# Kernel tuning notes

Measured on AMD Instinct MI355X. Metric: run time of the kernel, lower is better.

The kernel has to match this reference:

```python
import jax, jax.numpy as jnp
import numpy as np

D_MODEL = 512
H = 8
DEPTH = D_MODEL // H
TOPK = 16
TAU_HID = max(4, D_MODEL // 2)  # 256
TAU_EPS = 1e-6
DT = 1.0
T_SCALAR = 1.0  # default t in call()


def setup_inputs() -> dict:
    key = jax.random.key(0)
    ks = jax.random.split(key, 24)
    B, T = 2, 1024
    D2 = 2 * DEPTH

    def w(k, shape, fan_in):
        return jax.random.normal(k, shape, dtype=jnp.float32) / np.sqrt(fan_in)

    inp = {
        "x": jax.random.normal(ks[0], (B, T, D_MODEL), dtype=jnp.float32),
        "Wq": w(ks[1], (D_MODEL, D_MODEL), D_MODEL), "bq": jnp.zeros((D_MODEL,), jnp.float32),
        "Wk": w(ks[2], (D_MODEL, D_MODEL), D_MODEL), "bk": jnp.zeros((D_MODEL,), jnp.float32),
        "Wv": w(ks[3], (D_MODEL, D_MODEL), D_MODEL), "bv": jnp.zeros((D_MODEL,), jnp.float32),
        "Wo": w(ks[4], (D_MODEL, D_MODEL), D_MODEL), "bo": jnp.zeros((D_MODEL,), jnp.float32),
        "Wpi": w(ks[5], (D2, D_MODEL), D2), "bpi": jnp.zeros((D_MODEL,), jnp.float32),
        "Wpo": w(ks[6], (D_MODEL, 1), D_MODEL), "bpo": jnp.zeros((1,), jnp.float32),
        "Wta": w(ks[7], (D2, 1), D2), "bta": jnp.zeros((1,), jnp.float32),
        "Wtb": w(ks[8], (D2, 1), D2), "btb": jnp.zeros((1,), jnp.float32),
        "Wti": w(ks[9], (D2, TAU_HID), D2), "bti": jnp.zeros((TAU_HID,), jnp.float32),
        "Wto": w(ks[10], (TAU_HID, 1), TAU_HID), "bto": jnp.zeros((1,), jnp.float32),
    }
    return inp


def reference(x, Wq, bq, Wk, bk, Wv, bv, Wo, bo,
              Wpi, bpi, Wpo, bpo, Wta, bta, Wtb, btb, Wti, bti, Wto, bto):
    B, T, _ = x.shape

    def split_heads(z):
        return z.reshape(B, T, H, DEPTH).transpose(0, 2, 1, 3)  # [B,H,T,D]

    qh = split_heads(x @ Wq + bq)
    kh = split_heads(x @ Wk + bk)
    vh = split_heads(x @ Wv + bv)

    # top-k pairwise scores (q @ k^T), select K keys per query
    scores = jnp.einsum('bhqd,bhkd->bhqk', qh, kh)  # [B,H,T,T]
    _, idx = jax.lax.top_k(scores, TOPK)            # [B,H,T,K]

    # gather k and v at top-k indices -> [B,H,T,K,D]
    kg = jnp.take_along_axis(kh[:, :, None, :, :], idx[..., None], axis=3)
    vg = jnp.take_along_axis(vh[:, :, None, :, :], idx[..., None], axis=3)

    # per-pair features [q_i ; k_j] -> [B,H,T,K,2D]
    qt = jnp.broadcast_to(qh[:, :, :, None, :], (B, H, T, TOPK, DEPTH))
    pairs = jnp.concatenate([qt, kg], axis=-1)

    # phi: Dense(d_model) -> Dense(1) -> sigmoid
    phi = jax.nn.sigmoid(((pairs @ Wpi + bpi) @ Wpo + bpo)[..., 0])
    # time interpolation: sigmoid(a*t + b)
    t_a = (pairs @ Wta + bta)[..., 0]
    t_b = (pairs @ Wtb + btb)[..., 0]
    t_interp = jax.nn.sigmoid(t_a * T_SCALAR + t_b)
    # tau: Dense(d_model//2) -> Dense(1) -> softplus + eps
    tau = jax.nn.softplus(((pairs @ Wti + bti) @ Wto + bto)[..., 0]) + TAU_EPS

    # mode == 'exact'
    attn_logits = phi / tau * (1.0 - jnp.exp(-tau * t_interp))
    attn = jax.nn.softmax(attn_logits, axis=-1)  # [B,H,T,K]

    out_h = jnp.einsum('bhqk,bhqkd->bhqd', attn, vg) * DT  # [B,H,T,D]
    combined = out_h.transpose(0, 2, 1, 3).reshape(B, T, D_MODEL)
    return combined @ Wo + bo  # return_sequences=True
```

## Files before the change

### kernel.cpp

```cpp
#include <hip/hip_runtime.h>
#include <math.h>

#define BDIM 2
#define TT 1024
#define NH 8
#define HD 64
#define NTOPK 16
#define NBH 16
#define NTOK 16384

__global__ __launch_bounds__(256) void k_collapse64(
    const float* __restrict__ Wpi, const float* __restrict__ bpi,
    const float* __restrict__ Wpo, const float* __restrict__ bpo,
    const float* __restrict__ Wti, const float* __restrict__ bti,
    const float* __restrict__ Wto, const float* __restrict__ bto,
    double* __restrict__ wphid, double* __restrict__ wtaud,
    double* __restrict__ ccd) {
  int tid = threadIdx.x;
  int blk = blockIdx.x;
  if (blk < 16) {
    int r = blk * 16 + (tid >> 4);
    int l = tid & 15;
    double s = 0.;
    if (r < 128) {
      for (int i = 0; i < 32; ++i)
        s += (double)Wpi[r * 512 + l + 16 * i] * (double)Wpo[l + 16 * i];
    } else {
      int rr = r - 128;
      for (int i = 0; i < 16; ++i)
        s += (double)Wti[rr * 256 + l + 16 * i] * (double)Wto[l + 16 * i];
    }
#pragma unroll
    for (int off = 8; off >= 1; off >>= 1) s += __shfl_xor(s, off, 64);
    if (l == 0) {
      if (r < 128) wphid[r] = s;
      else wtaud[r - 128] = s;
    }
  } else {
    int lane = tid & 63;
    if (tid < 64) {
      double p = 0.;
      for (int c = lane; c < 512; c += 64) p += (double)bpi[c] * (double)Wpo[c];
#pragma unroll
      for (int off = 32; off >= 1; off >>= 1) p += __shfl_xor(p, off, 64);
      if (lane == 0) ccd[0] = p + (double)bpo[0];
    } else if (tid < 128) {
      double p = 0.;
      for (int c = lane; c < 256; c += 64) p += (double)bti[c] * (double)Wto[c];
#pragma unroll
      for (int off = 32; off >= 1; off >>= 1) p += __shfl_xor(p, off, 64);
      if (lane == 0) ccd[1] = p + (double)bto[0];
    }
  }
}

__device__ __forceinline__ void gemm_body(
    const float* __restrict__ A, const float* __restrict__ W,
    const float* __restrict__ bias, float* __restrict__ out,
    int bm, int bn, int mode) {
  __shared__ float As[16][64];
  __shared__ float Bs[16][64];
  const int tid = threadIdx.x;
  const int tx = tid & 15;
  const int ty = tid >> 4;
  const int lr = tid >> 2;
  const int lc = (tid & 3) << 2;
  float acc[4][4] = {{0.f, 0.f, 0.f, 0.f}};
  for (int k0 = 0; k0 < 512; k0 += 16) {
    float4 av = *(const float4*)&A[(bm + lr) * 512 + k0 + lc];
    As[lc + 0][lr] = av.x;
    As[lc + 1][lr] = av.y;
    As[lc + 2][lr] = av.z;
    As[lc + 3][lr] = av.w;
    *(float4*)&Bs[ty][tx << 2] = *(const float4*)&W[(k0 + ty) * 512 + bn + (tx << 2)];
    __syncthreads();
#pragma unroll
    for (int kk = 0; kk < 16; ++kk) {
      float4 a = *(const float4*)&As[kk][ty * 4];
      float4 b = *(const float4*)&Bs[kk][tx << 2];
      acc[0][0] = fmaf(a.x, b.x, acc[0][0]);
      acc[0][1] = fmaf(a.x, b.y, acc[0][1]);
      acc[0][2] = fmaf(a.x, b.z, acc[0][2]);
      acc[0][3] = fmaf(a.x, b.w, acc[0][3]);
      acc[1][0] = fmaf(a.y, b.x, acc[1][0]);
      acc[1][1] = fmaf(a.y, b.y, acc[1][1]);
      acc[1][2] = fmaf(a.y, b.z, acc[1][2]);
      acc[1][3] = fmaf(a.y, b.w, acc[1][3]);
      acc[2][0] = fmaf(a.z, b.x, acc[2][0]);
      acc[2][1] = fmaf(a.z, b.y, acc[2][1]);
      acc[2][2] = fmaf(a.z, b.z, acc[2][2]);
      acc[2][3] = fmaf(a.z, b.w, acc[2][3]);
      acc[3][0] = fmaf(a.w, b.x, acc[3][0]);
      acc[3][1] = fmaf(a.w, b.y, acc[3][1]);
      acc[3][2] = fmaf(a.w, b.z, acc[3][2]);
      acc[3][3] = fmaf(a.w, b.w, acc[3][3]);
    }
    __syncthreads();
  }
#pragma unroll
  for (int i = 0; i < 4; ++i) {
    int row = bm + ty * 4 + i;
    float4 r;
    r.x = acc[i][0] + bias[bn + tx * 4 + 0];
    r.y = acc[i][1] + bias[bn + tx * 4 + 1];
    r.z = acc[i][2] + bias[bn + tx * 4 + 2];
    r.w = acc[i][3] + bias[bn + tx * 4 + 3];
    if (mode == 0) {
      *(float4*)&out[row * 512 + bn + tx * 4] = r;
    } else {
      int bb = row >> 10;
      int tt2 = row & 1023;
      int head = bn >> 6;
      *(float4*)&out[(((bb * NH + head) * TT + tt2) << 6) + tx * 4] = r;
    }
  }
}

__global__ __launch_bounds__(256) void k_gemm(
    const float* __restrict__ A, const float* __restrict__ W,
    const float* __restrict__ bias, float* __restrict__ out, int mode) {
  gemm_body(A, W, bias, out, blockIdx.y * 64, blockIdx.x * 64, mode);
}

__global__ __launch_bounds__(256) void k_gemm_qkv(
    const float* __restrict__ A,
    const float* __restrict__ Wq, const float* __restrict__ bq,
    const float* __restrict__ Wk, const float* __restrict__ bk,
    const float* __restrict__ Wv, const float* __restrict__ bv,
    float* __restrict__ Qf, float* __restrict__ Kf, float* __restrict__ Vf) {
  int which = blockIdx.x >> 3;
  int bn = (blockIdx.x & 7) * 64;
  const float* W = (which == 0) ? Wq : (which == 1) ? Wk : Wv;
  const float* b = (which == 0) ? bq : (which == 1) ? bk : bv;
  float* out = (which == 0) ? Qf : (which == 1) ? Kf : Vf;
  gemm_body(A, W, b, out, blockIdx.y * 64, bn, 1);
}

__global__ __launch_bounds__(256) void k_tokscal64(
    const float* __restrict__ Qg, const float* __restrict__ Kg,
    const double* __restrict__ wphid, const float* __restrict__ Wta,
    const float* __restrict__ Wtb, const double* __restrict__ wtaud,
    double4* __restrict__ sqd4, double4* __restrict__ skd4) {
  __shared__ double wp[128], wa[128], wb[128], wt[128];
  int tid = threadIdx.x;
  if (tid < 128) {
    wp[tid] = wphid[tid];
    wa[tid] = (double)Wta[tid];
    wb[tid] = (double)Wtb[tid];
    wt[tid] = wtaud[tid];
  }
  __syncthreads();
  int tok = blockIdx.x * 256 + tid;
  const float* qr = Qg + (size_t)tok * 64;
  const float* kr = Kg + (size_t)tok * 64;
  double sp = 0., sa = 0., sb = 0., st = 0.;
  double kp = 0., ka = 0., kb2 = 0., kt = 0.;
#pragma unroll
  for (int d = 0; d < 64; ++d) {
    double q = (double)qr[d];
    double k = (double)kr[d];
    sp += q * wp[d];
    sa += q * wa[d];
    sb += q * wb[d];
    st += q * wt[d];
    kp += k * wp[64 + d];
    ka += k * wa[64 + d];
    kb2 += k * wb[64 + d];
    kt += k * wt[64 + d];
  }
  sqd4[tok] = make_double4(sp, sa, sb, st);
  skd4[tok] = make_double4(kp, ka, kb2, kt);
}

__global__ __launch_bounds__(256) void k_trans(
    const float* __restrict__ Kf, float* __restrict__ Kt) {
  __shared__ float tile[64][65];
  const int kt0 = blockIdx.x * 64;
  const int bh = blockIdx.y;
  const int t = threadIdx.x;
  const int rr = t >> 4;
  const int d4 = (t & 15) << 2;
#pragma unroll
  for (int i = 0; i < 4; ++i) {
    int row = i * 16 + rr;
    float4 v = *(const float4*)&Kf[((size_t)(bh * TT + kt0 + row)) * 64 + d4];
    tile[row][d4 + 0] = v.x;
    tile[row][d4 + 1] = v.y;
    tile[row][d4 + 2] = v.z;
    tile[row][d4 + 3] = v.w;
  }
  __syncthreads();
#pragma unroll
  for (int i = 0; i < 4; ++i) {
    int d = i * 16 + rr;
    int k4 = (t & 15) << 2;
    float4 v;
    v.x = tile[k4 + 0][d];
    v.y = tile[k4 + 1][d];
    v.z = tile[k4 + 2][d];
    v.w = tile[k4 + 3][d];
    *(float4*)&Kt[((size_t)(bh * 64 + d)) * 1024 + kt0 + k4] = v;
  }
}

__global__ __launch_bounds__(256) void k_score(
    const float* __restrict__ Qf, const float* __restrict__ Kt,
    float* __restrict__ Sc) {
  __shared__ float As[32][132];
  __shared__ float Bs[32][64];
  const int bn = blockIdx.x * 64;
  const int bm = blockIdx.y * 128;
  const int bh = blockIdx.z;
  const float* A = Qf + (size_t)bh * (TT * 64);
  const float* W = Kt + (size_t)bh * (64 * 1024);
  float* out = Sc + (size_t)bh * (TT * 1024);
  const int tid = threadIdx.x;
  const int tx = tid & 15;
  const int ty = tid >> 4;
  float acc[8][4];
#pragma unroll
  for (int i = 0; i < 8; ++i)
#pragma unroll
    for (int j = 0; j < 4; ++j) acc[i][j] = 0.f;
  for (int k0 = 0; k0 < 64; k0 += 32) {
#pragma unroll
    for (int i = 0; i < 4; ++i) {
      int idx = i * 256 + tid;
      int row = idx >> 3;
      int c4 = (idx & 7) << 2;
      float4 av = *(const float4*)&A[(size_t)(bm + row) * 64 + k0 + c4];
      As[c4 + 0][row] = av.x;
      As[c4 + 1][row] = av.y;
      As[c4 + 2][row] = av.z;
      As[c4 + 3][row] = av.w;
    }
#pragma unroll
    for (int i = 0; i < 2; ++i) {
      int idx = i * 256 + tid;
      int br = idx >> 4;
      int bc = (idx & 15) << 2;
      *(float4*)&Bs[br][bc] = *(const float4*)&W[(size_t)(k0 + br) * 1024 + bn + bc];
    }
    __syncthreads();
#pragma unroll
    for (int kk = 0; kk < 32; ++kk) {
      float4 alo = *(const float4*)&As[kk][ty * 8];
      float4 ahi = *(const float4*)&As[kk][ty * 8 + 4];
      float4 b = *(const float4*)&Bs[kk][tx << 2];
      acc[0][0] = fmaf(alo.x, b.x, acc[0][0]);
      acc[0][1] = fmaf(alo.x, b.y, acc[0][1]);
      acc[0][2] = fmaf(alo.x, b.z, acc[0][2]);
      acc[0][3] = fmaf(alo.x, b.w, acc[0][3]);
      acc[1][0] = fmaf(alo.y, b.x, acc[1][0]);
      acc[1][1] = fmaf(alo.y, b.y, acc[1][1]);
      acc[1][2] = fmaf(alo.y, b.z, acc[1][2]);
      acc[1][3] = fmaf(alo.y, b.w, acc[1][3]);
      acc[2][0] = fmaf(alo.z, b.x, acc[2][0]);
      acc[2][1] = fmaf(alo.z, b.y, acc[2][1]);
      acc[2][2] = fmaf(alo.z, b.z, acc[2][2]);
      acc[2][3] = fmaf(alo.z, b.w, acc[2][3]);
      acc[3][0] = fmaf(alo.w, b.x, acc[3][0]);
      acc[3][1] = fmaf(alo.w, b.y, acc[3][1]);
      acc[3][2] = fmaf(alo.w, b.z, acc[3][2]);
      acc[3][3] = fmaf(alo.w, b.w, acc[3][3]);
      acc[4][0] = fmaf(ahi.x, b.x, acc[4][0]);
      acc[4][1] = fmaf(ahi.x, b.y, acc[4][1]);
      acc[4][2] = fmaf(ahi.x, b.z, acc[4][2]);
      acc[4][3] = fmaf(ahi.x, b.w, acc[4][3]);
      acc[5][0] = fmaf(ahi.y, b.x, acc[5][0]);
      acc[5][1] = fmaf(ahi.y, b.y, acc[5][1]);
      acc[5][2] = fmaf(ahi.y, b.z, acc[5][2]);
      acc[5][3] = fmaf(ahi.y, b.w, acc[5][3]);
      acc[6][0] = fmaf(ahi.z, b.x, acc[6][0]);
      acc[6][1] = fmaf(ahi.z, b.y, acc[6][1]);
      acc[6][2] = fmaf(ahi.z, b.z, acc[6][2]);
      acc[6][3] = fmaf(ahi.z, b.w, acc[6][3]);
      acc[7][0] = fmaf(ahi.w, b.x, acc[7][0]);
      acc[7][1] = fmaf(ahi.w, b.y, acc[7][1]);
      acc[7][2] = fmaf(ahi.w, b.z, acc[7][2]);
      acc[7][3] = fmaf(ahi.w, b.w, acc[7][3]);
    }
    __syncthreads();
  }
#pragma unroll
  for (int i = 0; i < 8; ++i) {
    float4 r = make_float4(acc[i][0], acc[i][1], acc[i][2], acc[i][3]);
    *(float4*)&out[(size_t)(bm + ty * 8 + i) * 1024 + bn + (tx << 2)] = r;
  }
}

__global__ __launch_bounds__(256) void k_topk(
    const float* __restrict__ Sc, const float* __restrict__ Vg,
    const double4* __restrict__ sqd4, const double4* __restrict__ skd4,
    const double* __restrict__ ccd, const float* __restrict__ btaP,
    const float* __restrict__ btbP, float* __restrict__ C) {
  const int tid = threadIdx.x;
  const int lane = tid & 63;
  const int wv = tid >> 6;
  const int qg = blockIdx.x * 4 + wv;
  const int bh = qg >> 10;
  const int qa = qg & 1023;
  const int bb = bh >> 3;
  const int hh = bh & 7;
  const float* rowp = Sc + (size_t)qg * 1024;
  const float* Vbh = Vg + (size_t)bh * (TT * 64);

  float v[16];
#pragma unroll
  for (int j4 = 0; j4 < 4; ++j4) {
    float4 t = *(const float4*)&rowp[j4 * 256 + lane * 4];
    v[j4 * 4 + 0] = t.x;
    v[j4 * 4 + 1] = t.y;
    v[j4 * 4 + 2] = t.z;
    v[j4 * 4 + 3] = t.w;
  }
  float gv[4];
  int gj[4];
#pragma unroll
  for (int g = 0; g < 4; ++g) {
    gv[g] = v[4 * g];
    gj[g] = 4 * g;
#pragma unroll
    for (int e = 1; e < 4; ++e) {
      if (v[4 * g + e] > gv[g]) { gv[g] = v[4 * g + e]; gj[g] = 4 * g + e; }
    }
  }
  int myk = 0;
#pragma unroll 1
  for (int it = 0; it < NTOPK; ++it) {
    float bvv = gv[0];
    int bjj = gj[0];
#pragma unroll
    for (int g = 1; g < 4; ++g) {
      if (gv[g] > bvv) { bvv = gv[g]; bjj = gj[g]; }
    }
    int bj = ((bjj >> 2) << 8) + (lane << 2) + (bjj & 3);
#pragma unroll
    for (int off = 32; off >= 1; off >>= 1) {
      float ov = __shfl_xor(bvv, off, 64);
      int oj = __shfl_xor(bj, off, 64);
      if (ov > bvv || (ov == bvv && oj < bj)) { bvv = ov; bj = oj; }
    }
    if (lane == it) myk = bj;
    int owner = (bj >> 2) & 63;
    int slot = (((bj >> 8) << 2)) | (bj & 3);
    if (lane == owner) {
#pragma unroll
      for (int jj = 0; jj < 16; ++jj)
        if (jj == slot) v[jj] = -INFINITY;
      int g2 = slot >> 2;
#pragma unroll
      for (int g = 0; g < 4; ++g) {
        if (g == g2) {
          float ngv = v[4 * g];
          int ngj = 4 * g;
#pragma unroll
          for (int e = 1; e < 4; ++e) {
            if (v[4 * g + e] > ngv) { ngv = v[4 * g + e]; ngj = 4 * g + e; }
          }
          gv[g] = ngv;
          gj[g] = ngj;
        }
      }
    }
  }
  const double cphi = ccd[0];
  const double ctau = ccd[1];
  const double bta0 = (double)btaP[0];
  const double btb0 = (double)btbP[0];
  double4 sq = sqd4[qg];
  float logit = -INFINITY;
  if (lane < 16) {
    double4 sk = skd4[bh * TT + myk];
    float xs = (float)(sq.x + sk.x + cphi);
    float ta = (float)(sq.y + sk.y + bta0);
    float tb = (float)(sq.z + sk.z + btb0);
    float tl = (float)(sq.w + sk.w + ctau);
    float phi = 1.f / (1.f + __expf(-xs));
    float ti = 1.f / (1.f + __expf(-(ta + tb)));
    float tau = fmaxf(tl, 0.f) + log1pf(__expf(-fabsf(tl))) + 1e-6f;
    logit = phi / tau * (1.f - __expf(-tau * ti));
  }
  float m = logit;
#pragma unroll
  for (int off = 8; off >= 1; off >>= 1) m = fmaxf(m, __shfl_xor(m, off, 64));
  float e = (lane < 16) ? __expf(logit - m) : 0.f;
  float ssum = e;
#pragma unroll
  for (int off = 8; off >= 1; off >>= 1) ssum += __shfl_xor(ssum, off, 64);
  float w = e / ssum;
  float outv = 0.f;
#pragma unroll
  for (int k2 = 0; k2 < NTOPK; ++k2) {
    float wk = __shfl(w, k2, 64);
    int ik = __shfl(myk, k2, 64);
    outv = fmaf(wk, Vbh[(size_t)ik * 64 + lane], outv);
  }
  C[(bb * TT + qa) * 512 + hh * 64 + lane] = outv;
}

__global__ __launch_bounds__(256) void k_attn(
    const float* __restrict__ Qg, const float* __restrict__ Kg,
    const float* __restrict__ Vg, const double4* __restrict__ sqd4,
    const double4* __restrict__ skd4, const double* __restrict__ ccd,
    const float* __restrict__ btaP, const float* __restrict__ btbP,
    float* __restrict__ C) {
  __shared__ float qs[8][64];
  __shared__ float sc[8][1024];
  const int bh = blockIdx.y;
  const int q0 = blockIdx.x * 8;
  const int tid = threadIdx.x;
  const int lane = tid & 63;
  const int wv = tid >> 6;
  if (tid < 128) {
    int q = tid >> 4, d4 = (tid & 15) << 2;
    *(float4*)&qs[q][d4] = *(const float4*)&Qg[(size_t)(bh * TT + q0 + q) * 64 + d4];
  }
  __syncthreads();
#pragma unroll 1
  for (int c = 0; c < 4; ++c) {
    const int kb = (c * 4 + wv) * 64;
    const float* krow = &Kg[(size_t)(bh * TT + kb + lane) * 64];
    float4 kr[16];
#pragma unroll
    for (int i = 0; i < 16; ++i) kr[i] = *(const float4*)&krow[i * 4];
#pragma unroll
    for (int q = 0; q < 8; ++q) {
      float s = 0.f;
#pragma unroll
      for (int i = 0; i < 16; ++i) {
        float4 q4 = *(const float4*)&qs[q][i * 4];
        s = fmaf(q4.x, kr[i].x, s);
        s = fmaf(q4.y, kr[i].y, s);
        s = fmaf(q4.z, kr[i].z, s);
        s = fmaf(q4.w, kr[i].w, s);
      }
      sc[q][kb + lane] = s;
    }
  }
  __syncthreads();
  const double cphi = ccd[0];
  const double ctau = ccd[1];
  const double bta0 = (double)btaP[0];
  const double btb0 = (double)btbP[0];
  const int bb = bh >> 3;
  const int hh = bh & 7;
  const float* Vbh = Vg + (size_t)bh * (TT * 64);
#pragma unroll 1
  for (int qq = 0; qq < 2; ++qq) {
    const int ql = wv * 2 + qq;
    const int qa = q0 + ql;
    const float* rowp = &sc[ql][0];
    float v[16];
#pragma unroll
    for (int jj = 0; jj < 16; ++jj) v[jj] = rowp[jj * 64 + lane];
    float gv[4];
    int gj[4];
#pragma unroll
    for (int g = 0; g < 4; ++g) {
      gv[g] = v[4 * g];
      gj[g] = 4 * g;
#pragma unroll
      for (int e = 1; e < 4; ++e) {
        if (v[4 * g + e] > gv[g]) { gv[g] = v[4 * g + e]; gj[g] = 4 * g + e; }
      }
    }
    int myk = 0;
#pragma unroll 1
    for (int it = 0; it < NTOPK; ++it) {
      float bvv = gv[0];
      int bjj = gj[0];
#pragma unroll
      for (int g = 1; g < 4; ++g) {
        if (gv[g] > bvv) { bvv = gv[g]; bjj = gj[g]; }
      }
      int bj = bjj * 64 + lane;
#pragma unroll
      for (int off = 32; off >= 1; off >>= 1) {
        float ov = __shfl_xor(bvv, off, 64);
        int oj = __shfl_xor(bj, off, 64);
        if (ov > bvv || (ov == bvv && oj < bj)) { bvv = ov; bj = oj; }
      }
      if (lane == it) myk = bj;
      int owner = bj & 63;
      int slot = bj >> 6;
      if (lane == owner) {
#pragma unroll
        for (int jj = 0; jj < 16; ++jj)
          if (jj == slot) v[jj] = -INFINITY;
        int g2 = slot >> 2;
#pragma unroll
        for (int g = 0; g < 4; ++g) {
          if (g == g2) {
            float ngv = v[4 * g];
            int ngj = 4 * g;
#pragma unroll
            for (int e = 1; e < 4; ++e) {
              if (v[4 * g + e] > ngv) { ngv = v[4 * g + e]; ngj = 4 * g + e; }
            }
            gv[g] = ngv;
            gj[g] = ngj;
          }
        }
      }
    }
    double4 sq = sqd4[bh * TT + qa];
    double logit = -INFINITY;
    if (lane < 16) {
      double4 sk = skd4[bh * TT + myk];
      double phi = 1.0 / (1.0 + exp(-(sq.x + sk.x + cphi)));
      double ta = sq.y + sk.y + bta0;
      double tb = sq.z + sk.z + btb0;
      double ti = 1.0 / (1.0 + exp(-(ta * 1.0 + tb)));
      double tl = sq.w + sk.w + ctau;
      double tau = fmax(tl, 0.0) + log1p(exp(-fabs(tl))) + 1e-6;
      logit = phi / tau * (1.0 - exp(-tau * ti));
    }
    double m = logit;
#pragma unroll
    for (int off = 8; off >= 1; off >>= 1) {
      double om = __shfl_xor(m, off, 64);
      m = fmax(m, om);
    }
    double e = (lane < 16) ? exp(logit - m) : 0.0;
    double ssum = e;
#pragma unroll
    for (int off = 8; off >= 1; off >>= 1) ssum += __shfl_xor(ssum, off, 64);
    double w = e / ssum;
    double outv = 0.0;
#pragma unroll
    for (int k2 = 0; k2 < NTOPK; ++k2) {
      double wk = __shfl(w, k2, 64);
      int ik = __shfl(myk, k2, 64);
      outv += wk * (double)Vbh[(size_t)ik * 64 + lane];
    }
    C[(bb * TT + qa) * 512 + hh * 64 + lane] = (float)outv;
  }
}

extern "C" void kernel_launch(void* const* d_in, const int* in_sizes, int n_in,
                              void* d_out, int out_size, void* d_ws, size_t ws_size,
                              hipStream_t stream) {
  (void)in_sizes; (void)n_in; (void)out_size;
  const float* x   = (const float*)d_in[0];
  const float* Wq  = (const float*)d_in[1];
  const float* bq  = (const float*)d_in[2];
  const float* Wk  = (const float*)d_in[3];
  const float* bk  = (const float*)d_in[4];
  const float* Wv  = (const float*)d_in[5];
  const float* bv  = (const float*)d_in[6];
  const float* Wo  = (const float*)d_in[7];
  const float* bo  = (const float*)d_in[8];
  const float* Wpi = (const float*)d_in[9];
  const float* bpi = (const float*)d_in[10];
  const float* Wpo = (const float*)d_in[11];
  const float* bpo = (const float*)d_in[12];
  const float* Wta = (const float*)d_in[13];
  const float* bta = (const float*)d_in[14];
  const float* Wtb = (const float*)d_in[15];
  const float* btb = (const float*)d_in[16];
  const float* Wti = (const float*)d_in[17];
  const float* bti = (const float*)d_in[18];
  const float* Wto = (const float*)d_in[19];
  const float* bto = (const float*)d_in[20];

  double* wsd = (double*)d_ws;
  double4* sqd4 = (double4*)wsd;
  double4* skd4 = (double4*)(wsd + 65536);
  double* wphid = wsd + 131072;
  double* wtaud = wsd + 131200;
  double* ccd   = wsd + 131328;
  float* fs = (float*)(wsd + 131332);
  float* Qf = fs;
  float* Kf = fs + 1048576;
  float* Vf = fs + 2097152;
  float* Cf = fs + 3145728;
  float* Kt = fs + 4194304;
  float* Sc = fs + 5242880;
  const size_t need = (size_t)131332 * 8 + (size_t)(5242880 + 16777216) * 4;

  hipLaunchKernelGGL(k_collapse64, dim3(17), dim3(256), 0, stream,
                     Wpi, bpi, Wpo, bpo, Wti, bti, Wto, bto, wphid, wtaud, ccd);
  hipLaunchKernelGGL(k_gemm_qkv, dim3(24, 32), dim3(256), 0, stream,
                     x, Wq, bq, Wk, bk, Wv, bv, Qf, Kf, Vf);
  hipLaunchKernelGGL(k_tokscal64, dim3(NTOK / 256), dim3(256), 0, stream,
                     Qf, Kf, wphid, Wta, Wtb, wtaud, sqd4, skd4);
  if (ws_size >= need) {
    hipLaunchKernelGGL(k_trans, dim3(16, 16), dim3(256), 0, stream, Kf, Kt);
    hipLaunchKernelGGL(k_score, dim3(16, 8, 16), dim3(256), 0, stream, Qf, Kt, Sc);
    hipLaunchKernelGGL(k_topk, dim3(NTOK / 4), dim3(256), 0, stream,
                       Sc, Vf, sqd4, skd4, ccd, bta, btb, Cf);
  } else {
    hipLaunchKernelGGL(k_attn, dim3(TT / 8, NBH), dim3(256), 0, stream,
                       Qf, Kf, Vf, sqd4, skd4, ccd, bta, btb, Cf);
  }
  hipLaunchKernelGGL(k_gemm, dim3(8, 32), dim3(256), 0, stream,
                     Cf, Wo, bo, (float*)d_out, 0);
}
```

Measured before the change: 276.0 us.

## Drop K transpose kernel, load K directly into larger score tiles, widen GEMM k-step

Removes the separate K transpose kernel; the score kernel now loads K rows directly and transposes them into shared memory, cutting one launch and a full round trip of K through global memory. The score tile grows from 128x64 to 128x128, with an 8x8 accumulator per thread to raise reuse, at the cost of more registers. The shared gemm body now steps k by 32 instead of 16 and pads the A tile, halving the number of barriers. The workspace layout shrinks because Kt is gone.

```diff
diff --git a/kernel.cpp b/kernel.cpp
--- a/kernel.cpp
+++ b/kernel.cpp
@@ -58,24 +58,34 @@
     const float* __restrict__ A, const float* __restrict__ W,
     const float* __restrict__ bias, float* __restrict__ out,
     int bm, int bn, int mode) {
-  __shared__ float As[16][64];
-  __shared__ float Bs[16][64];
+  __shared__ float As[32][68];
+  __shared__ float Bs[32][64];
   const int tid = threadIdx.x;
   const int tx = tid & 15;
   const int ty = tid >> 4;
-  const int lr = tid >> 2;
-  const int lc = (tid & 3) << 2;
   float acc[4][4] = {{0.f, 0.f, 0.f, 0.f}};
-  for (int k0 = 0; k0 < 512; k0 += 16) {
-    float4 av = *(const float4*)&A[(bm + lr) * 512 + k0 + lc];
-    As[lc + 0][lr] = av.x;
-    As[lc + 1][lr] = av.y;
-    As[lc + 2][lr] = av.z;
-    As[lc + 3][lr] = av.w;
-    *(float4*)&Bs[ty][tx << 2] = *(const float4*)&W[(k0 + ty) * 512 + bn + (tx << 2)];
+  for (int k0 = 0; k0 < 512; k0 += 32) {
+#pragma unroll
+    for (int i = 0; i < 2; ++i) {
+      int idx = i * 256 + tid;
+      int row = idx >> 3;
+      int c4 = (idx & 7) << 2;
+      float4 av = *(const float4*)&A[(bm + row) * 512 + k0 + c4];
+      As[c4 + 0][row] = av.x;
+      As[c4 + 1][row] = av.y;
+      As[c4 + 2][row] = av.z;
+      As[c4 + 3][row] = av.w;
+    }
+#pragma unroll
+    for (int i = 0; i < 2; ++i) {
+      int idx = i * 256 + tid;
+      int br = idx >> 4;
+      int bc = (idx & 15) << 2;
+      *(float4*)&Bs[br][bc] = *(const float4*)&W[(k0 + br) * 512 + bn + bc];
+    }
     __syncthreads();
 #pragma unroll
-    for (int kk = 0; kk < 16; ++kk) {
+    for (int kk = 0; kk < 32; ++kk) {
       float4 a = *(const float4*)&As[kk][ty * 4];
       float4 b = *(const float4*)&Bs[kk][tx << 2];
       acc[0][0] = fmaf(a.x, b.x, acc[0][0]);
@@ -172,56 +182,25 @@
   skd4[tok] = make_double4(kp, ka, kb2, kt);
 }
 
-__global__ __launch_bounds__(256) void k_trans(
-    const float* __restrict__ Kf, float* __restrict__ Kt) {
-  __shared__ float tile[64][65];
-  const int kt0 = blockIdx.x * 64;
-  const int bh = blockIdx.y;
-  const int t = threadIdx.x;
-  const int rr = t >> 4;
-  const int d4 = (t & 15) << 2;
-#pragma unroll
-  for (int i = 0; i < 4; ++i) {
-    int row = i * 16 + rr;
-    float4 v = *(const float4*)&Kf[((size_t)(bh * TT + kt0 + row)) * 64 + d4];
-    tile[row][d4 + 0] = v.x;
-    tile[row][d4 + 1] = v.y;
-    tile[row][d4 + 2] = v.z;
-    tile[row][d4 + 3] = v.w;
-  }
-  __syncthreads();
-#pragma unroll
-  for (int i = 0; i < 4; ++i) {
-    int d = i * 16 + rr;
-    int k4 = (t & 15) << 2;
-    float4 v;
-    v.x = tile[k4 + 0][d];
-    v.y = tile[k4 + 1][d];
-    v.z = tile[k4 + 2][d];
-    v.w = tile[k4 + 3][d];
-    *(float4*)&Kt[((size_t)(bh * 64 + d)) * 1024 + kt0 + k4] = v;
-  }
-}
-
 __global__ __launch_bounds__(256) void k_score(
-    const float* __restrict__ Qf, const float* __restrict__ Kt,
+    const float* __restrict__ Qf, const float* __restrict__ Kf,
     float* __restrict__ Sc) {
   __shared__ float As[32][132];
-  __shared__ float Bs[32][64];
-  const int bn = blockIdx.x * 64;
+  __shared__ float Bs[32][132];
+  const int bn = blockIdx.x * 128;
   const int bm = blockIdx.y * 128;
   const int bh = blockIdx.z;
   const float* A = Qf + (size_t)bh * (TT * 64);
-  const float* W = Kt + (size_t)bh * (64 * 1024);
+  const float* K = Kf + (size_t)bh * (TT * 64);
   float* out = Sc + (size_t)bh * (TT * 1024);
   const int tid = threadIdx.x;
   const int tx = tid & 15;
   const int ty = tid >> 4;
-  float acc[8][4];
+  float acc[8][8];
 #pragma unroll
   for (int i = 0; i < 8; ++i)
 #pragma unroll
-    for (int j = 0; j < 4; ++j) acc[i][j] = 0.f;
+    for (int j = 0; j < 8; ++j) acc[i][j] = 0.f;
   for (int k0 = 0; k0 < 64; k0 += 32) {
 #pragma unroll
     for (int i = 0; i < 4; ++i) {
@@ -233,59 +212,36 @@
       As[c4 + 1][row] = av.y;
       As[c4 + 2][row] = av.z;
       As[c4 + 3][row] = av.w;
-    }
-#pragma unroll
-    for (int i = 0; i < 2; ++i) {
-      int idx = i * 256 + tid;
-      int br = idx >> 4;
-      int bc = (idx & 15) << 2;
-      *(float4*)&Bs[br][bc] = *(const float4*)&W[(size_t)(k0 + br) * 1024 + bn + bc];
+      float4 kv = *(const float4*)&K[(size_t)(bn + row) * 64 + k0 + c4];
+      Bs[c4 + 0][row] = kv.x;
+      Bs[c4 + 1][row] = kv.y;
+      Bs[c4 + 2][row] = kv.z;
+      Bs[c4 + 3][row] = kv.w;
     }
     __syncthreads();
 #pragma unroll
     for (int kk = 0; kk < 32; ++kk) {
       float4 alo = *(const float4*)&As[kk][ty * 8];
       float4 ahi = *(const float4*)&As[kk][ty * 8 + 4];
-      float4 b = *(const float4*)&Bs[kk][tx << 2];
-      acc[0][0] = fmaf(alo.x, b.x, acc[0][0]);
-      acc[0][1] = fmaf(alo.x, b.y, acc[0][1]);
-      acc[0][2] = fmaf(alo.x, b.z, acc[0][2]);
-      acc[0][3] = fmaf(alo.x, b.w, acc[0][3]);
-      acc[1][0] = fmaf(alo.y, b.x, acc[1][0]);
-      acc[1][1] = fmaf(alo.y, b.y, acc[1][1]);
-      acc[1][2] = fmaf(alo.y, b.z, acc[1][2]);
-      acc[1][3] = fmaf(alo.y, b.w, acc[1][3]);
-      acc[2][0] = fmaf(alo.z, b.x, acc[2][0]);
-      acc[2][1] = fmaf(alo.z, b.y, acc[2][1]);
-      acc[2][2] = fmaf(alo.z, b.z, acc[2][2]);
-      acc[2][3] = fmaf(alo.z, b.w, acc[2][3]);
-      acc[3][0] = fmaf(alo.w, b.x, acc[3][0]);
-      acc[3][1] = fmaf(alo.w, b.y, acc[3][1]);
-      acc[3][2] = fmaf(alo.w, b.z, acc[3][2]);
-      acc[3][3] = fmaf(alo.w, b.w, acc[3][3]);
-      acc[4][0] = fmaf(ahi.x, b.x, acc[4][0]);
-      acc[4][1] = fmaf(ahi.x, b.y, acc[4][1]);
-      acc[4][2] = fmaf(ahi.x, b.z, acc[4][2]);
-      acc[4][3] = fmaf(ahi.x, b.w, acc[4][3]);
-      acc[5][0] = fmaf(ahi.y, b.x, acc[5][0]);
-      acc[5][1] = fmaf(ahi.y, b.y, acc[5][1]);
-      acc[5][2] = fmaf(ahi.y, b.z, acc[5][2]);
-      acc[5][3] = fmaf(ahi.y, b.w, acc[5][3]);
-      acc[6][0] = fmaf(ahi.z, b.x, acc[6][0]);
-      acc[6][1] = fmaf(ahi.z, b.y, acc[6][1]);
-      acc[6][2] = fmaf(ahi.z, b.z, acc[6][2]);
-      acc[6][3] = fmaf(ahi.z, b.w, acc[6][3]);
-      acc[7][0] = fmaf(ahi.w, b.x, acc[7][0]);
-      acc[7][1] = fmaf(ahi.w, b.y, acc[7][1]);
-      acc[7][2] = fmaf(ahi.w, b.z, acc[7][2]);
-      acc[7][3] = fmaf(ahi.w, b.w, acc[7][3]);
+      float4 blo = *(const float4*)&Bs[kk][tx * 8];
+      float4 bhi = *(const float4*)&Bs[kk][tx * 8 + 4];
+      float a[8] = {alo.x, alo.y, alo.z, alo.w, ahi.x, ahi.y, ahi.z, ahi.w};
+      float b[8] = {blo.x, blo.y, blo.z, blo.w, bhi.x, bhi.y, bhi.z, bhi.w};
+#pragma unroll
+      for (int i = 0; i < 8; ++i)
+#pragma unroll
+        for (int j = 0; j < 8; ++j)
+          acc[i][j] = fmaf(a[i], b[j], acc[i][j]);
     }
     __syncthreads();
   }
 #pragma unroll
   for (int i = 0; i < 8; ++i) {
-    float4 r = make_float4(acc[i][0], acc[i][1], acc[i][2], acc[i][3]);
-    *(float4*)&out[(size_t)(bm + ty * 8 + i) * 1024 + bn + (tx << 2)] = r;
+    float4 r0 = make_float4(acc[i][0], acc[i][1], acc[i][2], acc[i][3]);
+    float4 r1 = make_float4(acc[i][4], acc[i][5], acc[i][6], acc[i][7]);
+    size_t base = (size_t)(bm + ty * 8 + i) * 1024 + bn + tx * 8;
+    *(float4*)&out[base] = r0;
+    *(float4*)&out[base + 4] = r1;
   }
 }
 
@@ -575,9 +531,8 @@
   float* Kf = fs + 1048576;
   float* Vf = fs + 2097152;
   float* Cf = fs + 3145728;
-  float* Kt = fs + 4194304;
-  float* Sc = fs + 5242880;
-  const size_t need = (size_t)131332 * 8 + (size_t)(5242880 + 16777216) * 4;
+  float* Sc = fs + 4194304;
+  const size_t need = (size_t)131332 * 8 + (size_t)(4194304 + 16777216) * 4;
 
   hipLaunchKernelGGL(k_collapse64, dim3(17), dim3(256), 0, stream,
                      Wpi, bpi, Wpo, bpo, Wti, bti, Wto, bto, wphid, wtaud, ccd);
@@ -586,8 +541,7 @@
   hipLaunchKernelGGL(k_tokscal64, dim3(NTOK / 256), dim3(256), 0, stream,
                      Qf, Kf, wphid, Wta, Wtb, wtaud, sqd4, skd4);
   if (ws_size >= need) {
-    hipLaunchKernelGGL(k_trans, dim3(16, 16), dim3(256), 0, stream, Kf, Kt);
-    hipLaunchKernelGGL(k_score, dim3(16, 8, 16), dim3(256), 0, stream, Qf, Kt, Sc);
+    hipLaunchKernelGGL(k_score, dim3(8, 8, 16), dim3(256), 0, stream, Qf, Kf, Sc);
     hipLaunchKernelGGL(k_topk, dim3(NTOK / 4), dim3(256), 0, stream,
                        Sc, Vf, sqd4, skd4, ccd, bta, btb, Cf);
   } else {
```

After: 272.8 us. Within noise of the previous version (-1.2%).
